# Performance work log

Hardware: AMD Instinct MI355X
Metric: run time of the kernel (lower is better)

## Reference

```python
import jax, jax.numpy as jnp
import numpy as np

NEG_SLOPE = 0.2  # both GATConv internal LeakyReLU and the module-level activation


def gat_conv(x, src, dst, W, a_src, a_dst, bias):
    """PyG GATConv (concat=True, add_self_loops handled by caller via src/dst).
    x: [N, Din]; W: [Din, H*C]; a_src, a_dst: [H, C]; bias: [H*C]."""
    N = x.shape[0]
    H, C = a_src.shape
    h = (x @ W).reshape(N, H, C)                       # [N, H, C]
    al_src = jnp.einsum('nhc,hc->nh', h, a_src)        # [N, H]
    al_dst = jnp.einsum('nhc,hc->nh', h, a_dst)        # [N, H]
    e = jax.nn.leaky_relu(al_src[src] + al_dst[dst], NEG_SLOPE)  # [E, H]
    # segment softmax over edges grouped by destination node
    m = jax.ops.segment_max(e, dst, num_segments=N)    # [N, H]
    ex = jnp.exp(e - m[dst])
    denom = jax.ops.segment_sum(ex, dst, num_segments=N)
    alpha = ex / denom[dst]                            # [E, H]
    out = jax.ops.segment_sum(alpha[:, :, None] * h[src], dst, num_segments=N)
    return out.reshape(N, H * C) + bias


def setup_inputs() -> dict:
    key = jax.random.key(0)
    N, E = 50000, 800000
    D_IN, HID, H = 128, 128, 2
    C = HID // H
    ks = jax.random.split(key, 20)
    inp = {
        'x': jax.random.normal(ks[0], (N, D_IN), dtype=jnp.float32),
        'edge_index': jax.random.randint(ks[1], (2, E), 0, N, dtype=jnp.int64),
    }
    dims = [D_IN, HID, HID]  # input dims of the 3 GATConv layers
    for i, din in enumerate(dims, start=1):
        s = 1.0 / np.sqrt(din)
        inp[f'W{i}'] = jax.random.normal(ks[2 + 4 * i], (din, HID), dtype=jnp.float32) * s
        inp[f'a_src{i}'] = jax.random.normal(ks[3 + 4 * i], (H, C), dtype=jnp.float32) * 0.1
        inp[f'a_dst{i}'] = jax.random.normal(ks[4 + 4 * i], (H, C), dtype=jnp.float32) * 0.1
        inp[f'b{i}'] = jnp.zeros((HID,), dtype=jnp.float32)
    inp['lin_w'] = jax.random.normal(ks[2], (HID, 1), dtype=jnp.float32) * (1.0 / np.sqrt(HID))
    inp['lin_b'] = jnp.zeros((1,), dtype=jnp.float32)
    return inp


def reference(x, edge_index, W1, a_src1, a_dst1, b1, W2, a_src2, a_dst2, b2,
              W3, a_src3, a_dst3, b3, lin_w, lin_b):
    N = x.shape[0]
    loops = jnp.arange(N, dtype=edge_index.dtype)
    src = jnp.concatenate([edge_index[0], loops])  # add_self_loops=True
    dst = jnp.concatenate([edge_index[1], loops])

    h = jax.nn.leaky_relu(gat_conv(x, src, dst, W1, a_src1, a_dst1, b1), NEG_SLOPE)
    # dropout is identity in eval mode (p=0.0)
    h = jax.nn.leaky_relu(h + gat_conv(h, src, dst, W2, a_src2, a_dst2, b2), NEG_SLOPE)
    h = jax.nn.leaky_relu(h + gat_conv(h, src, dst, W3, a_src3, a_dst3, b3), NEG_SLOPE)
    logits = (h @ lin_w + lin_b).squeeze(-1)  # [N]
    return logits
```

## Files before the change

### kernel.cpp

```cpp
#include <hip/hip_runtime.h>
#include <hip/hip_bf16.h>
#include <hip/hip_fp16.h>

#define LEAK 0.2f
#define BCAP 4096

typedef _Float16 half8  __attribute__((ext_vector_type(8)));
typedef _Float16 half4v __attribute__((ext_vector_type(4)));
typedef float    float4v __attribute__((ext_vector_type(4)));


__global__ __launch_bounds__(256) void k_binscatter(const int* __restrict__ esrc,
                                                    const int* __restrict__ edst,
                                                    int* __restrict__ gcnt,
                                                    unsigned int* __restrict__ binned,
                                                    int E, int ETOT, int NBK, int eb,
                                                    const float* __restrict__ W0,
                                                    const float* __restrict__ W1,
                                                    const float* __restrict__ W2,
                                                    _Float16* __restrict__ w16t) {
    int t = threadIdx.x;
    if (blockIdx.x >= eb) {
        __shared__ _Float16 tile[64][68];
        int bb = blockIdx.x - eb;
        int m = bb >> 2;
        int ti = (bb >> 1) & 1, tj = bb & 1;
        const float* src = (m == 0) ? W0 : (m == 1 ? W1 : W2);
        _Float16* dst = w16t + m * 16384;
        for (int idx = t; idx < 4096; idx += 256) {
            int r = idx >> 6, c = idx & 63;
            tile[r][c] = (_Float16)src[(ti * 64 + r) * 128 + tj * 64 + c];
        }
        __syncthreads();
        for (int idx = t; idx < 4096; idx += 256) {
            int c = idx >> 6, r = idx & 63;
            dst[(tj * 64 + c) * 128 + ti * 64 + r] = tile[r][c];
        }
        return;
    }
    __shared__ int lh[512];
    __shared__ int lbase[512];
    for (int b = t; b < NBK; b += 256) lh[b] = 0;
    __syncthreads();
    int base = blockIdx.x * 4096;
    unsigned int word[16]; int bb[16], rk[16];
    #pragma unroll
    for (int u = 0; u < 16; ++u) {
        int e = base + u * 256 + t;
        bb[u] = -1;
        if (e < ETOT) {
            int s, d;
            if (e < E) { s = esrc[e]; d = edst[e]; } else { s = d = e - E; }
            int b = d >> 7;
            bb[u] = b;
            rk[u] = atomicAdd(&lh[b], 1);
            word[u] = (unsigned int)s | ((unsigned int)(d & 127) << 17);
        }
    }
    __syncthreads();
    for (int b = t; b < NBK; b += 256) {
        int c = lh[b];
        lbase[b] = c ? atomicAdd(&gcnt[b], c) : 0;
    }
    __syncthreads();
    #pragma unroll
    for (int u = 0; u < 16; ++u)
        if (bb[u] >= 0)
            binned[(size_t)bb[u] * BCAP + lbase[bb[u]] + rk[u]] = word[u];
}

__device__ void scatter2_body(int b, const unsigned int* __restrict__ binned,
                              const int* __restrict__ gcnt,
                              int2* __restrict__ offend,
                              int* __restrict__ csr, int N) {
    __shared__ int deg[128];
    __shared__ int lcur[128];
    __shared__ int wt[2];
    int t = threadIdx.x;
    int n0 = b << 7;
    if (t < 128) deg[t] = 0;
    __syncthreads();
    int beg = b * BCAP, end = beg + gcnt[b];
    for (int i = beg + t; i < end; i += 256)
        atomicAdd(&deg[binned[i] >> 17], 1);
    __syncthreads();
    int v = 0, x = 0;
    if (t < 128) {
        v = deg[t];
        x = v;
        int lane = t & 63;
        #pragma unroll
        for (int o = 1; o < 64; o <<= 1) {
            int y = __shfl_up(x, o);
            if (lane >= o) x += y;
        }
        if (lane == 63) wt[t >> 6] = x;
    }
    __syncthreads();
    if (t < 128) {
        int excl = x - v + ((t >= 64) ? wt[0] : 0) + beg;
        lcur[t] = excl;
        int node = n0 + t;
        if (node < N) offend[node] = make_int2(excl, excl + v);
    }
    __syncthreads();
    for (int i = beg + t; i < end; i += 256) {
        unsigned int u = binned[i];
        int pos = atomicAdd(&lcur[u >> 17], 1);
        csr[pos] = (int)(u & 0x1FFFF);
    }
}


__global__ __launch_bounds__(256) void k_gemm_mfma(const void* __restrict__ Xv, int xfp16,
                                                   const _Float16* __restrict__ WhT,
                                                   const float* __restrict__ a_src,
                                                   const float* __restrict__ a_dst,
                                                   _Float16* __restrict__ Hout,
                                                   float* __restrict__ alsrc,
                                                   float* __restrict__ aldst, int N,
                                                   int gemm_nb,
                                                   const unsigned int* __restrict__ binned,
                                                   const int* __restrict__ gcnt,
                                                   int2* __restrict__ offend,
                                                   int* __restrict__ csr) {
    if ((int)blockIdx.x >= gemm_nb) {
        scatter2_body((int)blockIdx.x - gemm_nb, binned, gcnt, offend, csr, N);
        return;
    }
    __shared__ _Float16 As[64][136];
    __shared__ float sS[64][2];
    __shared__ float sD[64][2];
    const int t = threadIdx.x;
    const int lane = t & 63, w = t >> 6;
    const int block_row = blockIdx.x * 64;

    if (t < 128) { sS[t >> 1][t & 1] = 0.f; sD[t >> 1][t & 1] = 0.f; }

    if (xfp16) {
        const _Float16* Xh = (const _Float16*)Xv;
        #pragma unroll
        for (int it = 0; it < 4; ++it) {
            int i = t + 256 * it;
            int row = i >> 4, c8 = i & 15;
            int gr = block_row + row;
            half8 hv = (half8){0,0,0,0,0,0,0,0};
            if (gr < N) hv = *(const half8*)(Xh + (size_t)gr * 128 + c8 * 8);
            *(half8*)(&As[row][c8 * 8]) = hv;
        }
    } else {
        const float* X = (const float*)Xv;
        #pragma unroll
        for (int it = 0; it < 8; ++it) {
            int i = t + 256 * it;
            int row = i >> 5, c4 = i & 31;
            int gr = block_row + row;
            float4 xv = make_float4(0.f, 0.f, 0.f, 0.f);
            if (gr < N) xv = *(const float4*)(X + (size_t)gr * 128 + c4 * 4);
            half4v hv;
            hv[0] = (_Float16)xv.x; hv[1] = (_Float16)xv.y;
            hv[2] = (_Float16)xv.z; hv[3] = (_Float16)xv.w;
            *(half4v*)(&As[row][c4 * 4]) = hv;
        }
    }

    const int l15 = lane & 15, kq = (lane >> 4) * 8;
    half8 bf[2][4];
    #pragma unroll
    for (int ntl = 0; ntl < 2; ++ntl) {
        int n0 = (w * 2 + ntl) * 16 + l15;
        #pragma unroll
        for (int kt = 0; kt < 4; ++kt)
            bf[ntl][kt] = *(const half8*)(WhT + (size_t)n0 * 128 + kt * 32 + kq);
    }
    __syncthreads();

    float4v acc[4][2];
    #pragma unroll
    for (int mt = 0; mt < 4; ++mt)
        #pragma unroll
        for (int ntl = 0; ntl < 2; ++ntl)
            acc[mt][ntl] = (float4v){0.f, 0.f, 0.f, 0.f};

    #pragma unroll
    for (int kt = 0; kt < 4; ++kt) {
        half8 a[4];
        #pragma unroll
        for (int mt = 0; mt < 4; ++mt)
            a[mt] = *(const half8*)(&As[mt * 16 + l15][kt * 32 + kq]);
        #pragma unroll
        for (int mt = 0; mt < 4; ++mt)
            #pragma unroll
            for (int ntl = 0; ntl < 2; ++ntl)
                acc[mt][ntl] = __builtin_amdgcn_mfma_f32_16x16x32_f16(
                    a[mt], bf[ntl][kt], acc[mt][ntl], 0, 0, 0);
    }

    #pragma unroll
    for (int mt = 0; mt < 4; ++mt) {
        int r0 = block_row + mt * 16 + (lane >> 4) * 4;
        #pragma unroll
        for (int ntl = 0; ntl < 2; ++ntl) {
            int col = (w * 2 + ntl) * 16 + l15;
            #pragma unroll
            for (int reg = 0; reg < 4; ++reg) {
                int r = r0 + reg;
                if (r < N) Hout[(size_t)r * 128 + col] = (_Float16)acc[mt][ntl][reg];
            }
        }
    }

    {
        int c0 = w * 32 + l15, c1 = c0 + 16;
        float as0 = a_src[c0], as1 = a_src[c1];
        float ad0 = a_dst[c0], ad1 = a_dst[c1];
        int head = w >> 1;
        #pragma unroll
        for (int mt = 0; mt < 4; ++mt) {
            #pragma unroll
            for (int reg = 0; reg < 4; ++reg) {
                float ps = (float)acc[mt][0][reg] * as0 + (float)acc[mt][1][reg] * as1;
                float pd = (float)acc[mt][0][reg] * ad0 + (float)acc[mt][1][reg] * ad1;
                #pragma unroll
                for (int o = 1; o < 16; o <<= 1) {
                    ps += __shfl_xor(ps, o);
                    pd += __shfl_xor(pd, o);
                }
                if (l15 == 0) {
                    int row = mt * 16 + (lane >> 4) * 4 + reg;
                    atomicAdd(&sS[row][head], ps);
                    atomicAdd(&sD[row][head], pd);
                }
            }
        }
    }
    __syncthreads();
    if (t < 128) {
        int row = t >> 1, head = t & 1;
        int gr = block_row + row;
        if (gr < N) {
            alsrc[gr * 2 + head] = sS[row][head];
            aldst[gr * 2 + head] = sD[row][head];
        }
    }
}


__global__ __launch_bounds__(256) void k_aggregate(
        const _Float16* __restrict__ H16,
        const float* __restrict__ alsrc,
        const float* __restrict__ aldst,
        const int2* __restrict__ offend,
        const int* __restrict__ csr,
        const float* __restrict__ bias,
        const _Float16* __restrict__ prev,
        _Float16* __restrict__ Out,
        const float* __restrict__ lw, const float* __restrict__ lb,
        float* __restrict__ logits, int N, int mode) {
    int wglobal = (int)((blockIdx.x * 256 + threadIdx.x) >> 6);
    int lane = threadIdx.x & 63;
    if (wglobal * 2 >= N) return;
    int half = lane >> 5;
    int hl = lane & 31;
    int node = wglobal * 2 + half;
    bool active = node < N;
    int nodeC = active ? node : (N - 1);
    int2 oe = offend[nodeC];
    int beg = oe.x;
    int end = active ? oe.y : beg;
    float2 adv = *(const float2*)(aldst + (size_t)nodeC * 2);
    float ad0 = adv.x, ad1 = adv.y;

    int p = hl & 15;
    int q = hl >> 4;
    bool head0 = p < 8;
    const _Float16* hbase = H16 + p * 8;
    int hb = half << 5;

    float acc[8];
    #pragma unroll
    for (int k = 0; k < 8; ++k) acc[k] = 0.f;
    float dsum = 0.f;

    for (int base = beg; base < end; base += 32) {
        int i = base + hl;
        int s = 0; float w0 = 0.f, w1 = 0.f;
        if (i < end) {
            s = csr[i];
            float2 al = *(const float2*)(&alsrc[s * 2]);
            float e0 = al.x + ad0; e0 = e0 > 0.f ? e0 : LEAK * e0;
            float e1 = al.y + ad1; e1 = e1 > 0.f ? e1 : LEAK * e1;
            w0 = __expf(e0); w1 = __expf(e1);
        }
        int cnt = min(32, end - base);
        int iters = (cnt + 1) >> 1;
        int jj = 0;
        for (; jj + 8 <= iters; jj += 8) {
            int sl0 = hb + (jj << 1) + q;
            int sjv[8]; float wsv[8];
            #pragma unroll
            for (int u = 0; u < 8; ++u) {
                sjv[u] = __shfl(s, sl0 + 2 * u);
                float wa = __shfl(w0, sl0 + 2 * u);
                float wb = __shfl(w1, sl0 + 2 * u);
                wsv[u] = head0 ? wa : wb;
            }
            uint4 rv[8];
            #pragma unroll
            for (int u = 0; u < 8; ++u)
                rv[u] = *(const uint4*)(hbase + (size_t)sjv[u] * 128);
            #pragma unroll
            for (int u = 0; u < 8; ++u) {
                const _Float16* h = (const _Float16*)&rv[u];
                #pragma unroll
                for (int k = 0; k < 8; ++k) acc[k] += wsv[u] * (float)h[k];
                dsum += wsv[u];
            }
        }
        for (; jj + 4 <= iters; jj += 4) {
            int sl0 = hb + (jj << 1) + q;
            int sj0 = __shfl(s, sl0), sj1 = __shfl(s, sl0 + 2);
            int sj2 = __shfl(s, sl0 + 4), sj3 = __shfl(s, sl0 + 6);
            float w00 = __shfl(w0, sl0),     w10 = __shfl(w1, sl0);
            float w01 = __shfl(w0, sl0 + 2), w11 = __shfl(w1, sl0 + 2);
            float w02 = __shfl(w0, sl0 + 4), w12 = __shfl(w1, sl0 + 4);
            float w03 = __shfl(w0, sl0 + 6), w13 = __shfl(w1, sl0 + 6);
            float ws0 = head0 ? w00 : w10;
            float ws1 = head0 ? w01 : w11;
            float ws2 = head0 ? w02 : w12;
            float ws3 = head0 ? w03 : w13;
            uint4 r0 = *(const uint4*)(hbase + (size_t)sj0 * 128);
            uint4 r1 = *(const uint4*)(hbase + (size_t)sj1 * 128);
            uint4 r2 = *(const uint4*)(hbase + (size_t)sj2 * 128);
            uint4 r3 = *(const uint4*)(hbase + (size_t)sj3 * 128);
            const _Float16* h0 = (const _Float16*)&r0;
            const _Float16* h1 = (const _Float16*)&r1;
            const _Float16* h2 = (const _Float16*)&r2;
            const _Float16* h3 = (const _Float16*)&r3;
            #pragma unroll
            for (int k = 0; k < 8; ++k) acc[k] += ws0 * (float)h0[k];
            #pragma unroll
            for (int k = 0; k < 8; ++k) acc[k] += ws1 * (float)h1[k];
            #pragma unroll
            for (int k = 0; k < 8; ++k) acc[k] += ws2 * (float)h2[k];
            #pragma unroll
            for (int k = 0; k < 8; ++k) acc[k] += ws3 * (float)h3[k];
            dsum += (ws0 + ws1) + (ws2 + ws3);
        }
        for (; jj + 2 <= iters; jj += 2) {
            int sl0 = hb + (jj << 1) + q;
            int sj0 = __shfl(s, sl0), sj1 = __shfl(s, sl0 + 2);
            float w00 = __shfl(w0, sl0),     w10 = __shfl(w1, sl0);
            float w01 = __shfl(w0, sl0 + 2), w11 = __shfl(w1, sl0 + 2);
            float ws0 = head0 ? w00 : w10;
            float ws1 = head0 ? w01 : w11;
            uint4 r0 = *(const uint4*)(hbase + (size_t)sj0 * 128);
            uint4 r1 = *(const uint4*)(hbase + (size_t)sj1 * 128);
            const _Float16* h0 = (const _Float16*)&r0;
            const _Float16* h1 = (const _Float16*)&r1;
            #pragma unroll
            for (int k = 0; k < 8; ++k) acc[k] += ws0 * (float)h0[k];
            #pragma unroll
            for (int k = 0; k < 8; ++k) acc[k] += ws1 * (float)h1[k];
            dsum += ws0 + ws1;
        }
        if (jj < iters) {
            int sl = hb + (jj << 1) + q;
            int   sj = __shfl(s,  sl);
            float wa = __shfl(w0, sl);
            float wb = __shfl(w1, sl);
            float ws = head0 ? wa : wb;
            uint4 raw = *(const uint4*)(hbase + (size_t)sj * 128);
            const _Float16* h = (const _Float16*)&raw;
            #pragma unroll
            for (int k = 0; k < 8; ++k) acc[k] += ws * (float)h[k];
            dsum += ws;
        }
    }

    #pragma unroll
    for (int k = 0; k < 8; ++k) acc[k] += __shfl_xor(acc[k], 16);
    dsum += __shfl_xor(dsum, 16);

    if (q == 0 && active) {
        float inv = 1.f / dsum;
        int c0 = p * 8;
        float v[8];
        #pragma unroll
        for (int k = 0; k < 8; ++k) v[k] = acc[k] * inv + bias[c0 + k];
        if (mode >= 1) {
            half8 pv = *(const half8*)(prev + (size_t)node * 128 + c0);
            #pragma unroll
            for (int k = 0; k < 8; ++k) v[k] += (float)pv[k];
        }
        #pragma unroll
        for (int k = 0; k < 8; ++k) v[k] = v[k] > 0.f ? v[k] : LEAK * v[k];
        if (mode == 2) {
            float partial = 0.f;
            #pragma unroll
            for (int k = 0; k < 8; ++k) partial += v[k] * lw[c0 + k];
            partial += __shfl_xor(partial, 1);
            partial += __shfl_xor(partial, 2);
            partial += __shfl_xor(partial, 4);
            partial += __shfl_xor(partial, 8);
            if (hl == 0) logits[node] = partial + lb[0];
        } else {
            half8 ov;
            #pragma unroll
            for (int k = 0; k < 8; ++k) ov[k] = (_Float16)v[k];
            *(half8*)(Out + (size_t)node * 128 + c0) = ov;
        }
    }
}


extern "C" void kernel_launch(void* const* d_in, const int* in_sizes, int n_in,
                              void* d_out, int out_size, void* d_ws, size_t ws_size,
                              hipStream_t stream) {
    const float* x    = (const float*)d_in[0];
    const int*   edge = (const int*)d_in[1];
    const float* W[3]  = {(const float*)d_in[2], (const float*)d_in[6], (const float*)d_in[10]};
    const float* as[3] = {(const float*)d_in[3], (const float*)d_in[7], (const float*)d_in[11]};
    const float* ad[3] = {(const float*)d_in[4], (const float*)d_in[8], (const float*)d_in[12]};
    const float* bs[3] = {(const float*)d_in[5], (const float*)d_in[9], (const float*)d_in[13]};
    const float* lw = (const float*)d_in[14];
    const float* lb = (const float*)d_in[15];

    const int N    = in_sizes[0] / 128;
    const int E    = in_sizes[1] / 2;
    const int ETOT = E + N;
    const int NBK  = (N + 127) >> 7;

    char* base = (char*)d_ws;
    size_t o = 0;
    auto carve = [&](size_t bytes) {
        char* p = base + o;
        o = (o + bytes + 255) & ~(size_t)255;
        return p;
    };
    int2*     offend = (int2*)    carve((size_t)N * 8);
    int*      gcnt   = (int*)     carve((size_t)NBK * 4);
    unsigned* binned = (unsigned*)carve((size_t)NBK * BCAP * 4);
    int*      csr    = (int*)     carve((size_t)NBK * BCAP * 4);
    float*    alsrc  = (float*)   carve((size_t)N * 2 * 4);
    float*    aldst  = (float*)   carve((size_t)N * 2 * 4);
    _Float16* h16    = (_Float16*)carve((size_t)N * 128 * 2);
    _Float16* bufA   = (_Float16*)carve((size_t)N * 128 * 2);
    _Float16* bufB   = (_Float16*)carve((size_t)N * 128 * 2);
    _Float16* w16t   = (_Float16*)carve((size_t)3 * 16384 * 2);
    (void)ws_size; (void)n_in; (void)out_size;

    const int* esrc = edge;
    const int* edst = edge + E;

    int eb = (ETOT + 4095) / 4096;

    hipMemsetAsync(gcnt, 0, (size_t)NBK * 4, stream);

    k_binscatter<<<eb + 12, 256, 0, stream>>>(esrc, edst, gcnt, binned, E, ETOT, NBK, eb,
                                              W[0], W[1], W[2], w16t);

    int gemm_blocks = (N + 63) / 64;
    int agg_blocks  = (N + 7) / 8;

    k_gemm_mfma<<<gemm_blocks + NBK, 256, 0, stream>>>(x, 0, w16t, as[0], ad[0], h16,
                                                       alsrc, aldst, N, gemm_blocks,
                                                       binned, gcnt, offend, csr);
    k_aggregate<<<agg_blocks, 256, 0, stream>>>(h16, alsrc, aldst, offend, csr,
                                                bs[0], nullptr, bufA, lw, lb, nullptr, N, 0);
    k_gemm_mfma<<<gemm_blocks, 256, 0, stream>>>(bufA, 1, w16t + 16384, as[1], ad[1], h16,
                                                 alsrc, aldst, N, gemm_blocks,
                                                 binned, gcnt, offend, csr);
    k_aggregate<<<agg_blocks, 256, 0, stream>>>(h16, alsrc, aldst, offend, csr,
                                                bs[1], bufA, bufB, lw, lb, nullptr, N, 1);
    k_gemm_mfma<<<gemm_blocks, 256, 0, stream>>>(bufB, 1, w16t + 32768, as[2], ad[2], h16,
                                                 alsrc, aldst, N, gemm_blocks,
                                                 binned, gcnt, offend, csr);
    k_aggregate<<<agg_blocks, 256, 0, stream>>>(h16, alsrc, aldst, offend, csr,
                                                bs[2], bufB, nullptr, lw, lb, (float*)d_out, N, 2);
}
```

Measured before the change: 285.5 us.

## Sort CSR neighbor lists by source tile, schedule CSR blocks first, drop 8-wide unroll

The CSR build now counts and places edges per destination in eight source-index sub-buckets, so each node's neighbor list comes out roughly ordered by source range. The aim is better cache locality for the gathered feature rows during aggregation. The CSR-building blocks are moved to the start of the fused GEMM grid so they are dispatched before the GEMM blocks. The 8-way unrolled gather loop in aggregation is removed, leaving the 4-way loop, which trades memory-level parallelism for lower register pressure. Shared memory use and atomic contention in the CSR build grow a little.

```diff
diff --git a/kernel.cpp b/kernel.cpp
--- a/kernel.cpp
+++ b/kernel.cpp
@@ -4,6 +4,8 @@
 
 #define LEAK 0.2f
 #define BCAP 4096
+#define NTILE 8
+#define TSHIFT 13
 
 typedef _Float16 half8  __attribute__((ext_vector_type(8)));
 typedef _Float16 half4v __attribute__((ext_vector_type(4)));
@@ -73,20 +75,23 @@
                               const int* __restrict__ gcnt,
                               int2* __restrict__ offend,
                               int* __restrict__ csr, int N) {
-    __shared__ int deg[128];
-    __shared__ int lcur[128];
+    __shared__ int deg[128 * NTILE];
+    __shared__ int lcur[128 * NTILE];
     __shared__ int wt[2];
     int t = threadIdx.x;
     int n0 = b << 7;
-    if (t < 128) deg[t] = 0;
+    for (int i = t; i < 128 * NTILE; i += 256) deg[i] = 0;
     __syncthreads();
     int beg = b * BCAP, end = beg + gcnt[b];
-    for (int i = beg + t; i < end; i += 256)
-        atomicAdd(&deg[binned[i] >> 17], 1);
+    for (int i = beg + t; i < end; i += 256) {
+        unsigned int u = binned[i];
+        atomicAdd(&deg[(u >> 17) * NTILE + ((u & 0x1FFFF) >> TSHIFT)], 1);
+    }
     __syncthreads();
     int v = 0, x = 0;
     if (t < 128) {
-        v = deg[t];
+        #pragma unroll
+        for (int k = 0; k < NTILE; ++k) v += deg[t * NTILE + k];
         x = v;
         int lane = t & 63;
         #pragma unroll
@@ -99,14 +104,19 @@
     __syncthreads();
     if (t < 128) {
         int excl = x - v + ((t >= 64) ? wt[0] : 0) + beg;
-        lcur[t] = excl;
+        int run = excl;
+        #pragma unroll
+        for (int k = 0; k < NTILE; ++k) {
+            lcur[t * NTILE + k] = run;
+            run += deg[t * NTILE + k];
+        }
         int node = n0 + t;
         if (node < N) offend[node] = make_int2(excl, excl + v);
     }
     __syncthreads();
     for (int i = beg + t; i < end; i += 256) {
         unsigned int u = binned[i];
-        int pos = atomicAdd(&lcur[u >> 17], 1);
+        int pos = atomicAdd(&lcur[(u >> 17) * NTILE + ((u & 0x1FFFF) >> TSHIFT)], 1);
         csr[pos] = (int)(u & 0x1FFFF);
     }
 }
@@ -119,13 +129,13 @@
                                                    _Float16* __restrict__ Hout,
                                                    float* __restrict__ alsrc,
                                                    float* __restrict__ aldst, int N,
-                                                   int gemm_nb,
+                                                   int csr_nb,
                                                    const unsigned int* __restrict__ binned,
                                                    const int* __restrict__ gcnt,
                                                    int2* __restrict__ offend,
                                                    int* __restrict__ csr) {
-    if ((int)blockIdx.x >= gemm_nb) {
-        scatter2_body((int)blockIdx.x - gemm_nb, binned, gcnt, offend, csr, N);
+    if ((int)blockIdx.x < csr_nb) {
+        scatter2_body((int)blockIdx.x, binned, gcnt, offend, csr, N);
         return;
     }
     __shared__ _Float16 As[64][136];
@@ -133,7 +143,7 @@
     __shared__ float sD[64][2];
     const int t = threadIdx.x;
     const int lane = t & 63, w = t >> 6;
-    const int block_row = blockIdx.x * 64;
+    const int block_row = ((int)blockIdx.x - csr_nb) * 64;
 
     if (t < 128) { sS[t >> 1][t & 1] = 0.f; sD[t >> 1][t & 1] = 0.f; }
 
@@ -295,28 +305,6 @@
         int cnt = min(32, end - base);
         int iters = (cnt + 1) >> 1;
         int jj = 0;
-        for (; jj + 8 <= iters; jj += 8) {
-            int sl0 = hb + (jj << 1) + q;
-            int sjv[8]; float wsv[8];
-            #pragma unroll
-            for (int u = 0; u < 8; ++u) {
-                sjv[u] = __shfl(s, sl0 + 2 * u);
-                float wa = __shfl(w0, sl0 + 2 * u);
-                float wb = __shfl(w1, sl0 + 2 * u);
-                wsv[u] = head0 ? wa : wb;
-            }
-            uint4 rv[8];
-            #pragma unroll
-            for (int u = 0; u < 8; ++u)
-                rv[u] = *(const uint4*)(hbase + (size_t)sjv[u] * 128);
-            #pragma unroll
-            for (int u = 0; u < 8; ++u) {
-                const _Float16* h = (const _Float16*)&rv[u];
-                #pragma unroll
-                for (int k = 0; k < 8; ++k) acc[k] += wsv[u] * (float)h[k];
-                dsum += wsv[u];
-            }
-        }
         for (; jj + 4 <= iters; jj += 4) {
             int sl0 = hb + (jj << 1) + q;
             int sj0 = __shfl(s, sl0), sj1 = __shfl(s, sl0 + 2);
@@ -463,18 +451,18 @@
     int gemm_blocks = (N + 63) / 64;
     int agg_blocks  = (N + 7) / 8;
 
-    k_gemm_mfma<<<gemm_blocks + NBK, 256, 0, stream>>>(x, 0, w16t, as[0], ad[0], h16,
-                                                       alsrc, aldst, N, gemm_blocks,
+    k_gemm_mfma<<<NBK + gemm_blocks, 256, 0, stream>>>(x, 0, w16t, as[0], ad[0], h16,
+                                                       alsrc, aldst, N, NBK,
                                                        binned, gcnt, offend, csr);
     k_aggregate<<<agg_blocks, 256, 0, stream>>>(h16, alsrc, aldst, offend, csr,
                                                 bs[0], nullptr, bufA, lw, lb, nullptr, N, 0);
     k_gemm_mfma<<<gemm_blocks, 256, 0, stream>>>(bufA, 1, w16t + 16384, as[1], ad[1], h16,
-                                                 alsrc, aldst, N, gemm_blocks,
+                                                 alsrc, aldst, N, 0,
                                                  binned, gcnt, offend, csr);
     k_aggregate<<<agg_blocks, 256, 0, stream>>>(h16, alsrc, aldst, offend, csr,
                                                 bs[1], bufA, bufB, lw, lb, nullptr, N, 1);
     k_gemm_mfma<<<gemm_blocks, 256, 0, stream>>>(bufB, 1, w16t + 32768, as[2], ad[2], h16,
-                                                 alsrc, aldst, N, gemm_blocks,
+                                                 alsrc, aldst, N, 0,
                                                  binned, gcnt, offend, csr);
     k_aggregate<<<agg_blocks, 256, 0, stream>>>(h16, alsrc, aldst, offend, csr,
                                                 bs[2], bufB, nullptr, lw, lb, (float*)d_out, N, 2);
```

Result: faster. 269.8 us (-5.5%).
